# Performance work log

Hardware: AMD Instinct MI355X
Metric: run time of the kernel (lower is better)

The kernel has to match this reference:

```python
import jax, jax.numpy as jnp
import numpy as np

BN_EPS = 1e-5
W_BITS = 2
A_BITS = 2


def _quantize_k(x, k):
    # uniform quantization of x in [0,1] to k bits, straight-through estimator
    n = float(2 ** k - 1)
    q = jnp.round(x * n) / n
    return x + jax.lax.stop_gradient(q - x)


def _quant_weight(w, k):
    # DoReFa-style weight quantization to [-1, 1]
    t = jnp.tanh(w)
    t = t / (2.0 * jnp.max(jnp.abs(t))) + 0.5
    return 2.0 * _quantize_k(t, k) - 1.0


def _quant_act(x, k):
    # DoReFa-style activation quantization: clamp to [0,1], quantize
    return _quantize_k(jnp.clip(x, 0.0, 1.0), k)


def _conv3x3(x, w, stride=1):
    # x: [N,C,H,W], w: [O,I,3,3], padding=1
    return jax.lax.conv_general_dilated(
        x, w, window_strides=(stride, stride), padding=((1, 1), (1, 1)),
        dimension_numbers=('NCHW', 'OIHW', 'NCHW'))


def _bn(x, gamma, beta, mean, var):
    inv = gamma / jnp.sqrt(var + BN_EPS)           # [C]
    return x * inv[None, :, None, None] + (beta - mean * inv)[None, :, None, None]


def setup_inputs() -> dict:
    key = jax.random.key(0)
    ks = jax.random.split(key, 8)
    N, C, H, W = 64, 256, 28, 28
    x = jax.random.normal(ks[0], (N, C, H, W), dtype=jnp.float32)
    w1 = jax.random.normal(ks[1], (C, C, 3, 3), dtype=jnp.float32) * 0.05
    w2 = jax.random.normal(ks[2], (C, C, 3, 3), dtype=jnp.float32) * 0.05
    g1 = jnp.ones((C,), jnp.float32)
    b1 = jnp.zeros((C,), jnp.float32)
    m1 = jax.random.normal(ks[3], (C,), dtype=jnp.float32) * 0.1
    v1 = jax.random.uniform(ks[4], (C,), dtype=jnp.float32) + 0.5
    g2 = jnp.ones((C,), jnp.float32)
    b2 = jnp.zeros((C,), jnp.float32)
    m2 = jax.random.normal(ks[5], (C,), dtype=jnp.float32) * 0.1
    v2 = jax.random.uniform(ks[6], (C,), dtype=jnp.float32) + 0.5
    return {'x': x, 'w1': w1, 'g1': g1, 'b1': b1, 'm1': m1, 'v1': v1,
            'w2': w2, 'g2': g2, 'b2': b2, 'm2': m2, 'v2': v2}


def reference(x, w1, g1, b1, m1, v1, w2, g2, b2, m2, v2):
    residual = x
    # conv1 (2-bit quantized weights & activations) -> bn1 -> relu
    out = _conv3x3(_quant_act(x, A_BITS), _quant_weight(w1, W_BITS), stride=1)
    out = jax.nn.relu(_bn(out, g1, b1, m1, v1))
    # conv2 (2-bit quantized) -> bn2
    out = _conv3x3(_quant_act(out, A_BITS), _quant_weight(w2, W_BITS), stride=1)
    out = _bn(out, g2, b2, m2, v2)
    # residual add + relu
    return jax.nn.relu(out + residual)
```

## Files before the change

kernel.cpp:

```cpp
#include <hip/hip_runtime.h>


#define ABUF 14745600
using i32x4 = __attribute__((ext_vector_type(4))) int;

__device__ __forceinline__ void gload16(const void* g, void* l) {
  typedef const __attribute__((address_space(1))) unsigned int* gp_t;
  typedef __attribute__((address_space(3))) unsigned int* lp_t;
  __builtin_amdgcn_global_load_lds((gp_t)g, (lp_t)l, 16, 0, 0);
}

__global__ void prep_bn(const float* g1, const float* b1, const float* m1, const float* v1,
                        const float* g2, const float* b2, const float* m2, const float* v2,
                        float* s1, float* t1, float* s2, float* t2) {
  int c = threadIdx.x;
  float i1 = g1[c] / sqrtf(v1[c] + 1e-5f);
  s1[c] = i1 * (1.f / 9.f);
  t1[c] = b1[c] - m1[c] * i1;
  float i2 = g2[c] / sqrtf(v2[c] + 1e-5f);
  s2[c] = i2 * (1.f / 9.f);
  t2[c] = b2[c] - m2[c] * i2;
}

__global__ void maxabs_k(const float* __restrict__ w1, const float* __restrict__ w2,
                         unsigned* mx) {
  const float4* v = (const float4*)(blockIdx.y ? w2 : w1);
  float loc = 0.f;
  for (int i = blockIdx.x * 256 + threadIdx.x; i < 147456; i += 65536) {
    float4 f = v[i];
    loc = fmaxf(loc, fmaxf(fmaxf(fabsf(f.x), fabsf(f.y)), fmaxf(fabsf(f.z), fabsf(f.w))));
  }
  #pragma unroll
  for (int off = 32; off; off >>= 1) loc = fmaxf(loc, __shfl_xor(loc, off));
  __shared__ float red[4];
  if ((threadIdx.x & 63) == 0) red[threadIdx.x >> 6] = loc;
  __syncthreads();
  if (threadIdx.x == 0) {
    loc = fmaxf(fmaxf(red[0], red[1]), fmaxf(red[2], red[3]));
    atomicMax(&mx[blockIdx.y], __float_as_uint(loc));
  }
}

__global__ void wquant_k(const float* __restrict__ w1, const float* __restrict__ w2,
                         const unsigned* __restrict__ mx,
                         signed char* __restrict__ wq1, signed char* __restrict__ wq2) {
  const float* w = blockIdx.y ? w2 : w1;
  signed char* o = blockIdx.y ? wq2 : wq1;
  int idx = blockIdx.x * 256 + threadIdx.x;
  int oo = idx / 2304, rr = idx % 2304, t9 = rr >> 8, ci = rr & 255;
  float mt = tanhf(__uint_as_float(mx[blockIdx.y]));
  float t = tanhf(w[oo * 2304 + ci * 9 + t9]) / (2.f * mt) + 0.5f;
  int q = (int)rintf(t * 3.f);
  o[idx] = (signed char)(2 * q - 3);
}

__global__ void border_zero(unsigned char* __restrict__ a1, unsigned char* __restrict__ a2) {
  int b = blockIdx.x;
  unsigned char* base = (b >= 64 ? a2 : a1) + (size_t)(b & 63) * 230400;
  int tid = threadIdx.x;
  #pragma unroll
  for (int it = 0; it < 8; ++it) {
    int pi = it * 16 + (tid >> 4);
    if (pi < 116) {
      int hh, ww;
      if (pi < 30)      { hh = 0;       ww = pi; }
      else if (pi < 60) { hh = 29;      ww = pi - 30; }
      else if (pi < 88) { hh = pi - 59; ww = 0; }
      else              { hh = pi - 87; ww = 29; }
      *(uint4*)(base + (hh * 30 + ww) * 256 + (tid & 15) * 16) = uint4{0, 0, 0, 0};
    }
  }
}

__global__ void aquant_k(const float* __restrict__ x, unsigned char* __restrict__ a1) {
  int n = blockIdx.x / 28, h = blockIdx.x % 28;
  __shared__ __align__(16) unsigned char l[28 * 256];
  int c = threadIdx.x;
  const float4* src = (const float4*)(x + (size_t)(n * 256 + c) * 784 + h * 28);
  #pragma unroll
  for (int i = 0; i < 7; ++i) {
    float4 f = src[i];
    int p = i * 4;
    l[(p + 0) * 256 + c] = (unsigned char)(int)rintf(3.f * fminf(fmaxf(f.x, 0.f), 1.f));
    l[(p + 1) * 256 + c] = (unsigned char)(int)rintf(3.f * fminf(fmaxf(f.y, 0.f), 1.f));
    l[(p + 2) * 256 + c] = (unsigned char)(int)rintf(3.f * fminf(fmaxf(f.z, 0.f), 1.f));
    l[(p + 3) * 256 + c] = (unsigned char)(int)rintf(3.f * fminf(fmaxf(f.w, 0.f), 1.f));
  }
  __syncthreads();
  if (threadIdx.x < 224) {
    int p = threadIdx.x >> 3, q = threadIdx.x & 7;
    const uint4* s = (const uint4*)&l[p * 256 + q * 32];
    uint4 v0 = s[0], v1 = s[1];
    unsigned char* dst = a1 + ((size_t)((n * 30 + h + 1) * 30) + (p + 1)) * 256 + q * 32;
    ((uint4*)dst)[0] = v0;
    ((uint4*)dst)[1] = v1;
  }
}

#define PH_MID() do { __builtin_amdgcn_s_barrier(); \
  asm volatile("s_waitcnt lgkmcnt(0)" ::: "memory"); \
  __builtin_amdgcn_sched_barrier(0); \
  __builtin_amdgcn_s_setprio(1); } while (0)
#define PH_END() do { __builtin_amdgcn_s_setprio(0); \
  __builtin_amdgcn_s_barrier(); } while (0)
#define PH_ENDV(N) do { __builtin_amdgcn_s_setprio(0); \
  asm volatile("s_waitcnt vmcnt(" #N ")" ::: "memory"); \
  __builtin_amdgcn_sched_barrier(0); \
  __builtin_amdgcn_s_barrier(); } while (0)

template <int MODE>
__global__ __launch_bounds__(512, 2) void conv_gemm(
    const unsigned char* __restrict__ act, const signed char* __restrict__ wq,
    const float* __restrict__ sC, const float* __restrict__ tC,
    const float* __restrict__ xres, unsigned char* __restrict__ actout,
    float* __restrict__ fout) {
  extern __shared__ __align__(16) char lds[];
  const int tid = threadIdx.x, wv = tid >> 6, lane = tid & 63;
  const int pixBase = blockIdx.x * 256;
  const int wvm = wv >> 2, wvn = wv & 3;
  constexpr int RAoff = (MODE == 0) ? 0 : 32768;
  constexpr int RBoff = 32768 - RAoff;

  int pixB[2][2], wB[2][2];
  {
    int s = (lane & 7) ^ ((lane >> 3) & 7);
    #pragma unroll
    for (int h = 0; h < 2; ++h)
      #pragma unroll
      for (int c = 0; c < 2; ++c) {
        int r = h * 128 + c * 64 + wv * 8 + (lane >> 3);
        int p = pixBase + r;
        int n = p / 784, rem = p % 784, hh = rem / 28, ww = rem % 28;
        pixB[h][c] = (((n * 30 + hh) * 30 + ww) << 8) + (s << 4);
        wB[h][c] = r * 2304 + (s << 4);
      }
  }
  auto tof = [](int kt) {
    int tap = kt >> 1;
    return ((tap / 3) * 30 + (tap % 3)) * 256 + ((kt & 1) << 7);
  };
  auto stagePix = [&](int h, int kt) {
    const int base = (kt & 1) * 65536 + h * 16384 + wv * 1024;
    const int toff = tof(kt);
    gload16(act + pixB[h][0] + toff, &lds[base]);
    gload16(act + pixB[h][1] + toff, &lds[base + 8192]);
  };
  auto stageW = [&](int h, int kt) {
    const int base = (kt & 1) * 65536 + 32768 + h * 16384 + wv * 1024;
    gload16(wq + wB[h][0] + kt * 128, &lds[base]);
    gload16(wq + wB[h][1] + kt * 128, &lds[base + 8192]);
  };
  auto stageA = [&](int h, int kt) { if (MODE == 0) stagePix(h, kt); else stageW(h, kt); };
  auto stageB = [&](int h, int kt) { if (MODE == 0) stageW(h, kt); else stagePix(h, kt); };

  i32x4 acc[8][4];
  #pragma unroll
  for (int i = 0; i < 8; ++i)
    #pragma unroll
    for (int j = 0; j < 4; ++j) acc[i][j] = (i32x4){0, 0, 0, 0};
  i32x4 pa[4][2], pb0[2][2], pb1[2][2];

  auto rdA = [&](int buf, int mh) {
    #pragma unroll
    for (int f = 0; f < 4; ++f) {
      int r = wvm * 128 + mh * 64 + f * 16 + (lane & 15);
      int rb = buf * 65536 + RAoff + r * 128;
      #pragma unroll
      for (int kc = 0; kc < 2; ++kc) {
        int sl = kc * 4 + (lane >> 4);
        pa[f][kc] = *(const i32x4*)&lds[rb + ((sl ^ (r & 7)) << 4)];
      }
    }
  };
  auto rdB = [&](int buf, int nh, i32x4 (*pb)[2]) {
    #pragma unroll
    for (int g = 0; g < 2; ++g) {
      int r = wvn * 64 + nh * 32 + g * 16 + (lane & 15);
      int rb = buf * 65536 + RBoff + r * 128;
      #pragma unroll
      for (int kc = 0; kc < 2; ++kc) {
        int sl = kc * 4 + (lane >> 4);
        pb[g][kc] = *(const i32x4*)&lds[rb + ((sl ^ (r & 7)) << 4)];
      }
    }
  };
  auto quad = [&](int mh, int nh, i32x4 (*pb)[2]) {
    #pragma unroll
    for (int f = 0; f < 4; ++f)
      #pragma unroll
      for (int g = 0; g < 2; ++g)
        #pragma unroll
        for (int kc = 0; kc < 2; ++kc)
          acc[mh * 4 + f][nh * 2 + g] = __builtin_amdgcn_mfma_i32_16x16x64_i8(
              pa[f][kc], pb[g][kc], acc[mh * 4 + f][nh * 2 + g], 0, 0, 0);
  };

  stageB(0, 0); stageA(0, 0); stageB(1, 0); stageA(1, 0);
  stageB(0, 1); stageA(0, 1); stageB(1, 1);
  asm volatile("s_waitcnt vmcnt(6)" ::: "memory");
  __builtin_amdgcn_sched_barrier(0);
  __builtin_amdgcn_s_barrier();

  for (int it = 0; it < 9; ++it) {
    const int ktY = 2 * it + 1, ktX2 = 2 * it + 2, ktY2 = 2 * it + 3;
    const bool st = (it < 8);
    rdA(0, 0); rdB(0, 0, pb0);
    stageA(1, ktY);
    PH_MID(); quad(0, 0, pb0); PH_END();
    rdB(0, 1, pb1);
    PH_MID(); quad(0, 1, pb1); PH_END();
    rdA(0, 1);
    if (st) stageB(0, ktX2);
    PH_MID(); quad(1, 0, pb0); PH_END();
    if (st) { stageA(0, ktX2); stageB(1, ktX2); }
    PH_MID(); quad(1, 1, pb1);
    if (st) { PH_ENDV(6); } else { PH_ENDV(0); }
    rdA(1, 0); rdB(1, 0, pb0);
    if (st) stageA(1, ktX2);
    PH_MID(); quad(0, 0, pb0); PH_END();
    rdB(1, 1, pb1);
    PH_MID(); quad(0, 1, pb1); PH_END();
    rdA(1, 1);
    if (st) stageB(0, ktY2);
    PH_MID(); quad(1, 0, pb0); PH_END();
    if (st) { stageA(0, ktY2); stageB(1, ktY2); }
    PH_MID(); quad(1, 1, pb1);
    PH_ENDV(6);
  }

  if (MODE == 0) {
    float sj[4], tj[4];
    #pragma unroll
    for (int j = 0; j < 4; ++j) {
      int c = wvn * 64 + j * 16 + (lane & 15);
      sj[j] = sC[c]; tj[j] = tC[c];
    }
    __syncthreads();
    #pragma unroll
    for (int i = 0; i < 8; ++i) {
      int lp0 = wvm * 128 + i * 16 + ((lane >> 4) << 2);
      #pragma unroll
      for (int j = 0; j < 4; ++j) {
        int lch = wvn * 64 + j * 16 + (lane & 15);
        #pragma unroll
        for (int r = 0; r < 4; ++r) {
          float y = (float)acc[i][j][r] * sj[j] + tj[j];
          y = fminf(fmaxf(y, 0.f), 1.f);
          int lp = lp0 + r;
          lds[lp * 256 + (lch ^ ((lp & 7) << 4))] = (char)(int)rintf(y * 3.f);
        }
      }
    }
    __syncthreads();
    int rr = tid >> 1, hf = tid & 1;
    int p = pixBase + rr;
    int n = p / 784, rem = p % 784, hh = rem / 28, ww = rem % 28;
    unsigned char* dst = actout + (((n * 30 + hh + 1) * 30 + (ww + 1)) << 8) + hf * 128;
    #pragma unroll
    for (int k = 0; k < 8; ++k) {
      uint4 v = *(const uint4*)&lds[rr * 256 + ((hf * 128 + k * 16) ^ ((rr & 7) << 4))];
      *(uint4*)(dst + k * 16) = v;
    }
  } else {
    #pragma unroll
    for (int i = 0; i < 8; ++i) {
      #pragma unroll
      for (int r = 0; r < 4; ++r) {
        int c = wvm * 128 + i * 16 + ((lane >> 4) << 2) + r;
        float s = sC[c], t = tC[c];
        #pragma unroll
        for (int j = 0; j < 4; ++j) {
          int m = pixBase + wvn * 64 + j * 16 + (lane & 15);
          int n = m / 784, rem = m % 784;
          int addr = n * 200704 + c * 784 + rem;
          float y = (float)acc[i][j][r] * s + t + xres[addr];
          fout[addr] = fmaxf(y, 0.f);
        }
      }
    }
  }
}

extern "C" void kernel_launch(void* const* d_in, const int* in_sizes, int n_in,
                              void* d_out, int out_size, void* d_ws, size_t ws_size,
                              hipStream_t stream) {
  const float* x  = (const float*)d_in[0];
  const float* w1 = (const float*)d_in[1];
  const float* g1 = (const float*)d_in[2];
  const float* b1 = (const float*)d_in[3];
  const float* m1 = (const float*)d_in[4];
  const float* v1 = (const float*)d_in[5];
  const float* w2 = (const float*)d_in[6];
  const float* g2 = (const float*)d_in[7];
  const float* b2 = (const float*)d_in[8];
  const float* m2 = (const float*)d_in[9];
  const float* v2 = (const float*)d_in[10];

  char* ws = (char*)d_ws;
  unsigned* mx = (unsigned*)ws;
  float* s1 = (float*)(ws + 1024);
  float* t1 = (float*)(ws + 2048);
  float* s2 = (float*)(ws + 3072);
  float* t2 = (float*)(ws + 4096);
  unsigned char* a1 = (unsigned char*)(ws + 8192);
  unsigned char* a2 = a1 + ABUF;
  signed char* wq1 = (signed char*)(a2 + ABUF);
  signed char* wq2 = wq1 + 589824;

  void (*k0)(const unsigned char*, const signed char*, const float*, const float*,
             const float*, unsigned char*, float*) = conv_gemm<0>;
  void (*k1)(const unsigned char*, const signed char*, const float*, const float*,
             const float*, unsigned char*, float*) = conv_gemm<1>;
  hipFuncSetAttribute((const void*)k0, hipFuncAttributeMaxDynamicSharedMemorySize, 131072);
  hipFuncSetAttribute((const void*)k1, hipFuncAttributeMaxDynamicSharedMemorySize, 131072);

  hipMemsetAsync(ws, 0, 1024, stream);
  prep_bn<<<1, 256, 0, stream>>>(g1, b1, m1, v1, g2, b2, m2, v2, s1, t1, s2, t2);
  maxabs_k<<<dim3(256, 2), 256, 0, stream>>>(w1, w2, mx);
  wquant_k<<<dim3(2304, 2), 256, 0, stream>>>(w1, w2, mx, wq1, wq2);
  border_zero<<<128, 256, 0, stream>>>(a1, a2);
  aquant_k<<<64 * 28, 256, 0, stream>>>(x, a1);
  conv_gemm<0><<<196, 512, 131072, stream>>>(a1, wq1, s1, t1, nullptr, a2, nullptr);
  conv_gemm<1><<<196, 512, 131072, stream>>>(a2, wq2, s2, t2, x, nullptr, (float*)d_out);
}
```

Before: 224.7 us.

## Fuse prep kernels, coalesce activation quant and conv2 epilogue, swizzle block order

Folds the BN prep into the max-abs kernel and replaces the atomic max with per-block partials that wquant reduces itself, which removes a memset and a launch. Border zeroing moves into a rewritten activation-quant kernel that reads x with float4 along pixels and transposes through shared memory into packed channel bytes. The conv2 epilogue now stages accumulators through LDS so residual loads and output stores are float4 and coalesced along pixels. Conv blocks are remapped with an XCD-style swizzle, and the MFMA loop order is changed to put kc outermost. These changes cut launch count and uncoalesced global traffic, at the cost of extra LDS passes and barriers in the epilogue.

```diff
diff --git a/kernel.cpp b/kernel.cpp
--- a/kernel.cpp
+++ b/kernel.cpp
@@ -10,90 +10,112 @@
   __builtin_amdgcn_global_load_lds((gp_t)g, (lp_t)l, 16, 0, 0);
 }
 
-__global__ void prep_bn(const float* g1, const float* b1, const float* m1, const float* v1,
-                        const float* g2, const float* b2, const float* m2, const float* v2,
-                        float* s1, float* t1, float* s2, float* t2) {
-  int c = threadIdx.x;
-  float i1 = g1[c] / sqrtf(v1[c] + 1e-5f);
-  s1[c] = i1 * (1.f / 9.f);
-  t1[c] = b1[c] - m1[c] * i1;
-  float i2 = g2[c] / sqrtf(v2[c] + 1e-5f);
-  s2[c] = i2 * (1.f / 9.f);
-  t2[c] = b2[c] - m2[c] * i2;
-}
-
 __global__ void maxabs_k(const float* __restrict__ w1, const float* __restrict__ w2,
-                         unsigned* mx) {
-  const float4* v = (const float4*)(blockIdx.y ? w2 : w1);
+                         float* __restrict__ partial,
+                         const float* g1, const float* b1, const float* m1, const float* v1,
+                         const float* g2, const float* b2, const float* m2, const float* v2,
+                         float* s1, float* t1, float* s2, float* t2) {
+  int t = threadIdx.x, bx = blockIdx.x, ten = blockIdx.y;
+  if (ten == 0 && bx == 0) {
+    float i1 = g1[t] / sqrtf(v1[t] + 1e-5f);
+    s1[t] = i1 * (1.f / 9.f);
+    t1[t] = b1[t] - m1[t] * i1;
+    float i2 = g2[t] / sqrtf(v2[t] + 1e-5f);
+    s2[t] = i2 * (1.f / 9.f);
+    t2[t] = b2[t] - m2[t] * i2;
+  }
+  const float4* v = (const float4*)(ten ? w2 : w1);
   float loc = 0.f;
-  for (int i = blockIdx.x * 256 + threadIdx.x; i < 147456; i += 65536) {
+  for (int i = bx * 256 + t; i < 147456; i += 16384) {
     float4 f = v[i];
     loc = fmaxf(loc, fmaxf(fmaxf(fabsf(f.x), fabsf(f.y)), fmaxf(fabsf(f.z), fabsf(f.w))));
   }
   #pragma unroll
   for (int off = 32; off; off >>= 1) loc = fmaxf(loc, __shfl_xor(loc, off));
   __shared__ float red[4];
-  if ((threadIdx.x & 63) == 0) red[threadIdx.x >> 6] = loc;
+  if ((t & 63) == 0) red[t >> 6] = loc;
   __syncthreads();
-  if (threadIdx.x == 0) {
-    loc = fmaxf(fmaxf(red[0], red[1]), fmaxf(red[2], red[3]));
-    atomicMax(&mx[blockIdx.y], __float_as_uint(loc));
-  }
+  if (t == 0)
+    partial[ten * 64 + bx] = fmaxf(fmaxf(red[0], red[1]), fmaxf(red[2], red[3]));
 }
 
 __global__ void wquant_k(const float* __restrict__ w1, const float* __restrict__ w2,
-                         const unsigned* __restrict__ mx,
+                         const float* __restrict__ partial,
                          signed char* __restrict__ wq1, signed char* __restrict__ wq2) {
   const float* w = blockIdx.y ? w2 : w1;
   signed char* o = blockIdx.y ? wq2 : wq1;
+  float pm = partial[blockIdx.y * 64 + (threadIdx.x & 63)];
+  #pragma unroll
+  for (int off = 32; off; off >>= 1) pm = fmaxf(pm, __shfl_xor(pm, off));
+  float mt = tanhf(pm);
   int idx = blockIdx.x * 256 + threadIdx.x;
   int oo = idx / 2304, rr = idx % 2304, t9 = rr >> 8, ci = rr & 255;
-  float mt = tanhf(__uint_as_float(mx[blockIdx.y]));
   float t = tanhf(w[oo * 2304 + ci * 9 + t9]) / (2.f * mt) + 0.5f;
   int q = (int)rintf(t * 3.f);
   o[idx] = (signed char)(2 * q - 3);
 }
 
-__global__ void border_zero(unsigned char* __restrict__ a1, unsigned char* __restrict__ a2) {
-  int b = blockIdx.x;
-  unsigned char* base = (b >= 64 ? a2 : a1) + (size_t)(b & 63) * 230400;
-  int tid = threadIdx.x;
-  #pragma unroll
-  for (int it = 0; it < 8; ++it) {
-    int pi = it * 16 + (tid >> 4);
-    if (pi < 116) {
-      int hh, ww;
-      if (pi < 30)      { hh = 0;       ww = pi; }
-      else if (pi < 60) { hh = 29;      ww = pi - 30; }
-      else if (pi < 88) { hh = pi - 59; ww = 0; }
-      else              { hh = pi - 87; ww = 29; }
-      *(uint4*)(base + (hh * 30 + ww) * 256 + (tid & 15) * 16) = uint4{0, 0, 0, 0};
-    }
-  }
-}
-
-__global__ void aquant_k(const float* __restrict__ x, unsigned char* __restrict__ a1) {
-  int n = blockIdx.x / 28, h = blockIdx.x % 28;
-  __shared__ __align__(16) unsigned char l[28 * 256];
-  int c = threadIdx.x;
-  const float4* src = (const float4*)(x + (size_t)(n * 256 + c) * 784 + h * 28);
-  #pragma unroll
-  for (int i = 0; i < 7; ++i) {
-    float4 f = src[i];
-    int p = i * 4;
-    l[(p + 0) * 256 + c] = (unsigned char)(int)rintf(3.f * fminf(fmaxf(f.x, 0.f), 1.f));
-    l[(p + 1) * 256 + c] = (unsigned char)(int)rintf(3.f * fminf(fmaxf(f.y, 0.f), 1.f));
-    l[(p + 2) * 256 + c] = (unsigned char)(int)rintf(3.f * fminf(fmaxf(f.z, 0.f), 1.f));
-    l[(p + 3) * 256 + c] = (unsigned char)(int)rintf(3.f * fminf(fmaxf(f.w, 0.f), 1.f));
+__device__ __forceinline__ int border_pix(int bp) {
+  int hh, ww;
+  if (bp < 30)      { hh = 0;       ww = bp; }
+  else if (bp < 60) { hh = 29;      ww = bp - 30; }
+  else if (bp < 88) { hh = bp - 59; ww = 0; }
+  else              { hh = bp - 87; ww = 29; }
+  return hh * 30 + ww;
+}
+
+__global__ void aquant_k(const float* __restrict__ x, unsigned char* __restrict__ a1,
+                         unsigned char* __restrict__ a2) {
+  __shared__ unsigned au[784 * 17];
+  const int t = threadIdx.x;
+  const int n = blockIdx.x >> 2, cq = blockIdx.x & 3;
+  const int c4 = t >> 4, q = t & 15;
+
+  #pragma unroll
+  for (int m = 0; m < 2; ++m) {
+    int s2 = t + m * 256;
+    if (s2 < 464) {
+      int bp = s2 >> 2, quad = s2 & 3;
+      size_t off = ((size_t)n * 900 + border_pix(bp)) * 256 + cq * 64 + quad * 16;
+      uint4 z = {0, 0, 0, 0};
+      *(uint4*)(a1 + off) = z;
+      *(uint4*)(a2 + off) = z;
+    }
+  }
+
+  const float* xb = x + (size_t)n * 200704 + (cq * 64 + c4 * 4) * 784;
+  #pragma unroll
+  for (int k = 0; k < 13; ++k) {
+    int hw4 = q + k * 16;
+    if (hw4 < 196) {
+      unsigned b[4][4];
+      #pragma unroll
+      for (int i = 0; i < 4; ++i) {
+        float4 f = *(const float4*)(xb + i * 784 + hw4 * 4);
+        b[i][0] = (unsigned)(int)rintf(3.f * fminf(fmaxf(f.x, 0.f), 1.f));
+        b[i][1] = (unsigned)(int)rintf(3.f * fminf(fmaxf(f.y, 0.f), 1.f));
+        b[i][2] = (unsigned)(int)rintf(3.f * fminf(fmaxf(f.z, 0.f), 1.f));
+        b[i][3] = (unsigned)(int)rintf(3.f * fminf(fmaxf(f.w, 0.f), 1.f));
+      }
+      #pragma unroll
+      for (int j = 0; j < 4; ++j)
+        au[(hw4 * 4 + j) * 17 + c4] = b[0][j] | (b[1][j] << 8) | (b[2][j] << 16) | (b[3][j] << 24);
+    }
   }
   __syncthreads();
-  if (threadIdx.x < 224) {
-    int p = threadIdx.x >> 3, q = threadIdx.x & 7;
-    const uint4* s = (const uint4*)&l[p * 256 + q * 32];
-    uint4 v0 = s[0], v1 = s[1];
-    unsigned char* dst = a1 + ((size_t)((n * 30 + h + 1) * 30) + (p + 1)) * 256 + q * 32;
-    ((uint4*)dst)[0] = v0;
-    ((uint4*)dst)[1] = v1;
+  #pragma unroll
+  for (int m = 0; m < 13; ++m) {
+    int s = t + m * 256;
+    if (s < 3136) {
+      int pix = s >> 2, quad = s & 3;
+      uint4 v;
+      v.x = au[pix * 17 + quad * 4 + 0];
+      v.y = au[pix * 17 + quad * 4 + 1];
+      v.z = au[pix * 17 + quad * 4 + 2];
+      v.w = au[pix * 17 + quad * 4 + 3];
+      int hh = pix / 28, ww = pix - hh * 28;
+      *(uint4*)(a1 + (((n * 30 + hh + 1) * 30) + ww + 1) * 256 + cq * 64 + quad * 16) = v;
+    }
   }
 }
 
@@ -116,7 +138,9 @@
     float* __restrict__ fout) {
   extern __shared__ __align__(16) char lds[];
   const int tid = threadIdx.x, wv = tid >> 6, lane = tid & 63;
-  const int pixBase = blockIdx.x * 256;
+  const int bswz = blockIdx.x & 7, bloc = blockIdx.x >> 3;
+  const int wg = (bswz < 4 ? bswz * 25 : 100 + (bswz - 4) * 24) + bloc;
+  const int pixBase = wg * 256;
   const int wvm = wv >> 2, wvn = wv & 3;
   constexpr int RAoff = (MODE == 0) ? 0 : 32768;
   constexpr int RBoff = 32768 - RAoff;
@@ -186,11 +210,11 @@
   };
   auto quad = [&](int mh, int nh, i32x4 (*pb)[2]) {
     #pragma unroll
-    for (int f = 0; f < 4; ++f)
-      #pragma unroll
-      for (int g = 0; g < 2; ++g)
+    for (int kc = 0; kc < 2; ++kc)
+      #pragma unroll
+      for (int f = 0; f < 4; ++f)
         #pragma unroll
-        for (int kc = 0; kc < 2; ++kc)
+        for (int g = 0; g < 2; ++g)
           acc[mh * 4 + f][nh * 2 + g] = __builtin_amdgcn_mfma_i32_16x16x64_i8(
               pa[f][kc], pb[g][kc], acc[mh * 4 + f][nh * 2 + g], 0, 0, 0);
   };
@@ -262,20 +286,35 @@
       *(uint4*)(dst + k * 16) = v;
     }
   } else {
-    #pragma unroll
-    for (int i = 0; i < 8; ++i) {
-      #pragma unroll
-      for (int r = 0; r < 4; ++r) {
-        int c = wvm * 128 + i * 16 + ((lane >> 4) << 2) + r;
-        float s = sC[c], t = tC[c];
+    float* ldsf = (float*)lds;
+    const int half = tid >> 8, row = (tid >> 4) & 15, seg = tid & 15;
+    #pragma unroll
+    for (int s = 0; s < 8; ++s) {
+      float* dst = ldsf + (s & 1) * 8448 + wvm * 4224;
+      #pragma unroll
+      for (int j = 0; j < 4; ++j)
         #pragma unroll
-        for (int j = 0; j < 4; ++j) {
-          int m = pixBase + wvn * 64 + j * 16 + (lane & 15);
-          int n = m / 784, rem = m % 784;
-          int addr = n * 200704 + c * 784 + rem;
-          float y = (float)acc[i][j][r] * s + t + xres[addr];
-          fout[addr] = fmaxf(y, 0.f);
-        }
+        for (int r = 0; r < 4; ++r)
+          dst[(((lane >> 4) << 2) + r) * 264 + wvn * 64 + j * 16 + (lane & 15)] =
+              (float)acc[s][j][r];
+      __syncthreads();
+      int c = half * 128 + s * 16 + row;
+      float sc = sC[c], tc = tC[c];
+      const float* src = ldsf + (s & 1) * 8448 + half * 4224 + row * 264 + seg * 16;
+      const float* xrc = xres + (size_t)c * 784;
+      float* foc = fout + (size_t)c * 784;
+      #pragma unroll
+      for (int f = 0; f < 4; ++f) {
+        int p = pixBase + seg * 16 + f * 4;
+        int n = p / 784, rem = p - n * 784;
+        float4 v = *(const float4*)(src + f * 4);
+        float4 xr = *(const float4*)(xrc + n * 200704 + rem);
+        float4 y;
+        y.x = fmaxf(v.x * sc + tc + xr.x, 0.f);
+        y.y = fmaxf(v.y * sc + tc + xr.y, 0.f);
+        y.z = fmaxf(v.z * sc + tc + xr.z, 0.f);
+        y.w = fmaxf(v.w * sc + tc + xr.w, 0.f);
+        *(float4*)(foc + n * 200704 + rem) = y;
       }
     }
   }
@@ -297,7 +336,7 @@
   const float* v2 = (const float*)d_in[10];
 
   char* ws = (char*)d_ws;
-  unsigned* mx = (unsigned*)ws;
+  float* partial = (float*)ws;
   float* s1 = (float*)(ws + 1024);
   float* t1 = (float*)(ws + 2048);
   float* s2 = (float*)(ws + 3072);
@@ -314,12 +353,11 @@
   hipFuncSetAttribute((const void*)k0, hipFuncAttributeMaxDynamicSharedMemorySize, 131072);
   hipFuncSetAttribute((const void*)k1, hipFuncAttributeMaxDynamicSharedMemorySize, 131072);
 
-  hipMemsetAsync(ws, 0, 1024, stream);
-  prep_bn<<<1, 256, 0, stream>>>(g1, b1, m1, v1, g2, b2, m2, v2, s1, t1, s2, t2);
-  maxabs_k<<<dim3(256, 2), 256, 0, stream>>>(w1, w2, mx);
-  wquant_k<<<dim3(2304, 2), 256, 0, stream>>>(w1, w2, mx, wq1, wq2);
-  border_zero<<<128, 256, 0, stream>>>(a1, a2);
-  aquant_k<<<64 * 28, 256, 0, stream>>>(x, a1);
+  maxabs_k<<<dim3(64, 2), 256, 0, stream>>>(w1, w2, partial,
+                                            g1, b1, m1, v1, g2, b2, m2, v2,
+                                            s1, t1, s2, t2);
+  wquant_k<<<dim3(2304, 2), 256, 0, stream>>>(w1, w2, partial, wq1, wq2);
+  aquant_k<<<256, 256, 0, stream>>>(x, a1, a2);
   conv_gemm<0><<<196, 512, 131072, stream>>>(a1, wq1, s1, t1, nullptr, a2, nullptr);
   conv_gemm<1><<<196, 512, 131072, stream>>>(a2, wq2, s2, t2, x, nullptr, (float*)d_out);
 }
```

After: 221.1 us. Within noise of the previous version (-1.6%).
